# Kernel tuning notes

Hardware: AMD Instinct MI355X
Metric: run time of the kernel (lower is better)

Reference implementation:

```python
import jax, jax.numpy as jnp
import numpy as np

B, S, D, H = 2, 2048, 1024, 16
HD = D // H  # head_dim = 64


def setup_inputs() -> dict:
    key = jax.random.key(0)
    ks = jax.random.split(key, 12)
    s = 1.0 / np.sqrt(D)
    inp = {
        "query": jax.random.normal(ks[0], (B, S, D), jnp.float32),
        "key": jax.random.normal(ks[1], (B, S, D), jnp.float32),
        "value": jax.random.normal(ks[2], (B, S, D), jnp.float32),
        # causal mask, shape (B, S, S); 0 means masked
        "mask": jnp.broadcast_to(jnp.tril(jnp.ones((S, S), jnp.int32)), (B, S, S)),
        "Wq": jax.random.normal(ks[3], (D, D), jnp.float32) * s,
        "bq": jnp.zeros((D,), jnp.float32),
        "Wk": jax.random.normal(ks[4], (D, D), jnp.float32) * s,
        "bk": jnp.zeros((D,), jnp.float32),
        "Wv": jax.random.normal(ks[5], (D, D), jnp.float32) * s,
        "bv": jnp.zeros((D,), jnp.float32),
        "Wo": jax.random.normal(ks[6], (D, D), jnp.float32) * s,
        "bo": jnp.zeros((D,), jnp.float32),
    }
    return inp


def reference(query, key, value, mask, Wq, bq, Wk, bk, Wv, bv, Wo, bo):
    # QKV projections (nn.Linear: x @ W.T + b), split into heads -> (B, H, S, HD)
    def proj(x, W, b):
        return (x @ W.T + b).reshape(B, S, H, HD).transpose(0, 2, 1, 3)

    q = proj(query, Wq, bq)
    k = proj(key, Wk, bk)
    v = proj(value, Wv, bv)

    # scores: (B, H, S, S)
    scores = jnp.einsum("bhqd,bhkd->bhqk", q, k) / np.sqrt(HD).astype(np.float32)
    scores = jnp.where(mask[:, None, :, :] == 0, jnp.float32(-1e9), scores)
    attn = jax.nn.softmax(scores, axis=-1)
    # dropout is identity in eval mode
    ctx = jnp.einsum("bhqk,bhkd->bhqd", attn, v)  # (B, H, S, HD)
    ctx = ctx.transpose(0, 2, 1, 3).reshape(B, S, D)
    return ctx @ Wo.T + bo
```

## Files before the change

kernel.cpp:

```cpp
#include <hip/hip_runtime.h>
#include <hip/hip_bf16.h>
#include <stdint.h>


#define LOG2E 1.4426950408889634f

typedef __bf16 bf16x8 __attribute__((ext_vector_type(8)));
typedef float f32x4 __attribute__((ext_vector_type(4)));

__device__ __forceinline__ ushort f2bf(float f) {
  union { float f; uint32_t u; } v; v.f = f;
  uint32_t u = v.u + 0x7FFFu + ((v.u >> 16) & 1u);
  return (ushort)(u >> 16);
}
__device__ __forceinline__ uint32_t pack2(float a, float b) {
  return (uint32_t)f2bf(a) | ((uint32_t)f2bf(b) << 16);
}
__device__ __forceinline__ bf16x8 ld_frag(const ushort* p) {
  return __builtin_bit_cast(bf16x8, *(const uint4*)p);
}
__device__ __forceinline__ void gl_lds16(const void* g, void* l) {
  __builtin_amdgcn_global_load_lds(
      (const __attribute__((address_space(1))) void*)g,
      (__attribute__((address_space(3))) void*)l, 16, 0, 0);
}

template <int ROWS>
__device__ __forceinline__ void stage_tile(const ushort* src, int stride,
                                           ushort* dst, int wid, int lane) {
  const int rloc = lane >> 3;
  const int gsrc = (lane & 7) ^ (rloc & 7);
  constexpr int RW = ROWS / 4;
  const ushort* s = src + (size_t)(wid * RW + rloc) * stride + gsrc * 8;
#pragma unroll
  for (int j = 0; j < RW / 8; ++j)
    gl_lds16(s + (size_t)(j * 8) * stride, dst + (wid * RW + j * 8) * 64);
}
__device__ __forceinline__ int swz(int row, int gran) {
  return row * 64 + ((gran ^ (row & 7)) << 3);
}

__device__ __forceinline__ void cvt8(const float* s, ushort* d) {
  float4 f0 = ((const float4*)s)[0];
  float4 f1 = ((const float4*)s)[1];
  uint4 h;
  h.x = pack2(f0.x, f0.y); h.y = pack2(f0.z, f0.w);
  h.z = pack2(f1.x, f1.y); h.w = pack2(f1.z, f1.w);
  *(uint4*)d = h;
}

__global__ void cvt_all(const float* __restrict__ s0, const float* __restrict__ s1,
                        const float* __restrict__ s2, const float* __restrict__ s3,
                        const float* __restrict__ s4, const float* __restrict__ s5,
                        const float* __restrict__ s6, ushort* __restrict__ d0,
                        ushort* __restrict__ d1, ushort* __restrict__ d2,
                        ushort* __restrict__ d3, ushort* __restrict__ d4,
                        ushort* __restrict__ d5, ushort* __restrict__ d6) {
  int y = blockIdx.y;
  int n = (y < 3) ? (4096 * 1024) : (1024 * 1024);
  int i = (blockIdx.x * 256 + threadIdx.x) * 8;
  if (i >= n) return;
  const float* s; ushort* d;
  switch (y) {
    case 0: s = s0; d = d0; break;
    case 1: s = s1; d = d1; break;
    case 2: s = s2; d = d2; break;
    case 3: s = s3; d = d3; break;
    case 4: s = s4; d = d4; break;
    case 5: s = s5; d = d5; break;
    default: s = s6; d = d6; break;
  }
  cvt8(s + i, d + i);
}

template <int BN, bool OUT_BF16, bool PROJ3>
__global__ __launch_bounds__(256, 2) void gemm_bt(
    const ushort* __restrict__ A0, const ushort* __restrict__ A1, const ushort* __restrict__ A2,
    const ushort* __restrict__ W0, const ushort* __restrict__ W1, const ushort* __restrict__ W2,
    const float* __restrict__ b0, const float* __restrict__ b1, const float* __restrict__ b2,
    void* __restrict__ Y0, void* __restrict__ Y1, void* __restrict__ Y2,
    int Ndim, int Kdim) {
  __shared__ ushort Al[128 * 64];
  __shared__ ushort Bl[BN * 64];

  const int z = PROJ3 ? blockIdx.z : 0;
  const ushort* A = (z == 0) ? A0 : (z == 1) ? A1 : A2;
  const ushort* W = (z == 0) ? W0 : (z == 1) ? W1 : W2;
  const float* bias = (z == 0) ? b0 : (z == 1) ? b1 : b2;
  void* Yp = (z == 0) ? Y0 : (z == 1) ? Y1 : Y2;

  const int tid = threadIdx.x;
  const int wid = tid >> 6, lane = tid & 63;
  const int row0 = blockIdx.y * 128, col0 = blockIdx.x * BN;
  const int wr = wid >> 1, wc = wid & 1;
  const int lr = lane & 15, lg = lane >> 4;
  constexpr int NF = BN / 32;

  f32x4 acc[4][NF] = {};

  for (int k0 = 0; k0 < Kdim; k0 += 64) {
    stage_tile<128>(A + (size_t)row0 * Kdim + k0, Kdim, Al, wid, lane);
    stage_tile<BN>(W + (size_t)col0 * Kdim + k0, Kdim, Bl, wid, lane);
    __syncthreads();

#pragma unroll
    for (int kk = 0; kk < 2; ++kk) {
      bf16x8 af[4], bfr[NF];
#pragma unroll
      for (int m = 0; m < 4; ++m)
        af[m] = ld_frag(&Al[swz(wr * 64 + m * 16 + lr, kk * 4 + lg)]);
#pragma unroll
      for (int n = 0; n < NF; ++n)
        bfr[n] = ld_frag(&Bl[swz(wc * (BN / 2) + n * 16 + lr, kk * 4 + lg)]);
#pragma unroll
      for (int m = 0; m < 4; ++m)
#pragma unroll
        for (int n = 0; n < NF; ++n)
          acc[m][n] = __builtin_amdgcn_mfma_f32_16x16x32_bf16(af[m], bfr[n], acc[m][n], 0, 0, 0);
    }
    __syncthreads();
  }

#pragma unroll
  for (int n = 0; n < NF; ++n) {
    int col = col0 + wc * (BN / 2) + n * 16 + lr;
    float bv = bias[col];
#pragma unroll
    for (int m = 0; m < 4; ++m) {
#pragma unroll
      for (int r = 0; r < 4; ++r) {
        int row = row0 + wr * 64 + m * 16 + lg * 4 + r;
        float v = acc[m][n][r] + bv;
        if (OUT_BF16)
          ((ushort*)Yp)[(size_t)row * Ndim + col] = f2bf(v);
        else
          ((float*)Yp)[(size_t)row * Ndim + col] = v;
      }
    }
  }
}

__global__ __launch_bounds__(256, 2) void attn_kernel(
    const ushort* __restrict__ Qb, const ushort* __restrict__ Kb,
    const ushort* __restrict__ Vb, ushort* __restrict__ Cx) {
  __shared__ ushort Kl[2][64 * 64];
  __shared__ ushort Vt[64 * 64];
  __shared__ ushort Pl[4][16 * 64];

  const int tid = threadIdx.x;
  const int wid = tid >> 6, lane = tid & 63;
  const int lr = lane & 15, lg = lane >> 4;
  const int x = blockIdx.x;
  const int y = blockIdx.y;
  const int m8 = (x + (y & 7)) & 7;
  const int yh = y >> 3;
  const int qi = (yh == 0) ? m8 : (yh == 1) ? 15 - m8 : (yh == 2) ? 16 + m8 : 31 - m8;
  const int qb0 = qi * 64;
  const int b = x >> 4, h = x & 15;
  const size_t base = (size_t)b * 2048 * 1024 + h * 64;
  const int q0w = qb0 + wid * 16;
  const float SCL = 0.125f * LOG2E;

  bf16x8 qf[2];
  {
    const ushort* qs = Qb + base + (size_t)(q0w + lr) * 1024 + lg * 8;
    qf[0] = ld_frag(qs);
    qf[1] = ld_frag(qs + 32);
  }

  f32x4 O[4] = {};
  float m_reg = -1e30f, l_reg = 0.f;

  const int nt = qi + 1;
  const int vp = tid & 31;
  const int vc = tid >> 5;

  stage_tile<64>(Kb + base, 1024, Kl[0], wid, lane);
  uint4 va = *(const uint4*)(Vb + base + (size_t)(2 * vp) * 1024 + vc * 8);
  uint4 vb = *(const uint4*)(Vb + base + (size_t)(2 * vp + 1) * 1024 + vc * 8);

  for (int t = 0; t < nt; ++t) {
    const int kv0 = t * 64;
    {
      const ushort* pA = (const ushort*)&va;
      const ushort* pB = (const ushort*)&vb;
#pragma unroll
      for (int j = 0; j < 8; ++j) {
        int d = vc * 8 + j;
        int idx = d * 64 + (((vp >> 2) ^ j) << 3) + ((vp * 2) & 7);
        *(uint32_t*)&Vt[idx] = (uint32_t)pA[j] | ((uint32_t)pB[j] << 16);
      }
    }
    __syncthreads();

    if (t + 1 < nt) {
      stage_tile<64>(Kb + base + (size_t)(kv0 + 64) * 1024, 1024, Kl[(t + 1) & 1], wid, lane);
      va = *(const uint4*)(Vb + base + (size_t)(kv0 + 64 + 2 * vp) * 1024 + vc * 8);
      vb = *(const uint4*)(Vb + base + (size_t)(kv0 + 64 + 2 * vp + 1) * 1024 + vc * 8);
    }

    const bool dm = (t == nt - 1);
    const ushort* Kc = Kl[t & 1];

    f32x4 st[4];
#pragma unroll
    for (int cb = 0; cb < 4; ++cb) {
      if (kv0 + cb * 16 > q0w + 15) {
        st[cb] = f32x4{-1e30f, -1e30f, -1e30f, -1e30f};
        continue;
      }
      f32x4 a = {};
#pragma unroll
      for (int kk = 0; kk < 2; ++kk) {
        bf16x8 kfrag = ld_frag(&Kc[swz(cb * 16 + lr, kk * 4 + lg)]);
        a = __builtin_amdgcn_mfma_f32_16x16x32_bf16(kfrag, qf[kk], a, 0, 0, 0);
      }
#pragma unroll
      for (int r = 0; r < 4; ++r) {
        float s = a[r] * SCL;
        if (dm) {
          int kv = kv0 + cb * 16 + lg * 4 + r;
          if (kv > q0w + lr) s = -1e30f;
        }
        a[r] = s;
      }
      st[cb] = a;
    }

    float tmax = -1e30f;
#pragma unroll
    for (int cb = 0; cb < 4; ++cb) {
      float c01 = fmaxf(st[cb][0], st[cb][1]);
      float c23 = fmaxf(st[cb][2], st[cb][3]);
      tmax = fmaxf(tmax, fmaxf(c01, c23));
    }
    tmax = fmaxf(tmax, __shfl_xor(tmax, 16));
    tmax = fmaxf(tmax, __shfl_xor(tmax, 32));
    float mnew = fmaxf(m_reg, tmax);
    float alpha = exp2f(m_reg - mnew);
    m_reg = mnew;

    float ts = 0.f;
#pragma unroll
    for (int cb = 0; cb < 4; ++cb)
#pragma unroll
      for (int r = 0; r < 4; ++r) {
        float p = exp2f(st[cb][r] - mnew);
        st[cb][r] = p;
        ts += p;
      }
    ts += __shfl_xor(ts, 16);
    ts += __shfl_xor(ts, 32);
    l_reg = l_reg * alpha + ts;

    float aO[4];
#pragma unroll
    for (int r = 0; r < 4; ++r)
      aO[r] = __shfl(alpha, (lane & 48) | ((lane >> 2) & 12) | r);
#pragma unroll
    for (int n = 0; n < 4; ++n)
#pragma unroll
      for (int r = 0; r < 4; ++r) O[n][r] *= aO[r];

    ushort* pw = &Pl[wid][0];
#pragma unroll
    for (int cb = 0; cb < 4; ++cb) {
      int g = ((cb * 2 + (lg >> 1)) ^ (lr & 7)) << 3;
      int idx = lr * 64 + g + ((lg & 1) * 4);
      *(uint32_t*)&pw[idx] = pack2(st[cb][0], st[cb][1]);
      *(uint32_t*)&pw[idx + 2] = pack2(st[cb][2], st[cb][3]);
    }

#pragma unroll
    for (int kk = 0; kk < 2; ++kk) {
      bf16x8 pa = ld_frag(&pw[swz(lr, kk * 4 + lg)]);
#pragma unroll
      for (int n = 0; n < 4; ++n) {
        bf16x8 vfr = ld_frag(&Vt[swz(n * 16 + lr, kk * 4 + lg)]);
        O[n] = __builtin_amdgcn_mfma_f32_16x16x32_bf16(pa, vfr, O[n], 0, 0, 0);
      }
    }
    __syncthreads();
  }

#pragma unroll
  for (int r = 0; r < 4; ++r) {
    float ls = __shfl(l_reg, (lane & 48) | ((lane >> 2) & 12) | r);
    float inv = 1.f / ls;
    size_t row = (size_t)b * 2048 + q0w + lg * 4 + r;
#pragma unroll
    for (int n = 0; n < 4; ++n)
      Cx[row * 1024 + h * 64 + n * 16 + lr] = f2bf(O[n][r] * inv);
  }
}

extern "C" void kernel_launch(void* const* d_in, const int* in_sizes, int n_in,
                              void* d_out, int out_size, void* d_ws, size_t ws_size,
                              hipStream_t stream) {
  const float* query = (const float*)d_in[0];
  const float* key_i = (const float*)d_in[1];
  const float* value = (const float*)d_in[2];
  const float* Wq = (const float*)d_in[4];
  const float* bq = (const float*)d_in[5];
  const float* Wk = (const float*)d_in[6];
  const float* bk = (const float*)d_in[7];
  const float* Wv = (const float*)d_in[8];
  const float* bv = (const float*)d_in[9];
  const float* Wo = (const float*)d_in[10];
  const float* bo = (const float*)d_in[11];
  float* out = (float*)d_out;

  const size_t MD = (size_t)4096 * 1024;
  const size_t DD = (size_t)1024 * 1024;
  ushort* qbf = (ushort*)d_ws;
  ushort* kbf = qbf + MD;
  ushort* vbf = kbf + MD;
  ushort* Wqb = vbf + MD;
  ushort* Wkb = Wqb + DD;
  ushort* Wvb = Wkb + DD;
  ushort* Wob = Wvb + DD;
  ushort* Qb = Wob + DD;
  ushort* Kb = Qb + MD;
  ushort* Vb = Kb + MD;
  ushort* Cx = Vb + MD;

  cvt_all<<<dim3(2048, 7), 256, 0, stream>>>(query, key_i, value, Wq, Wk, Wv, Wo,
                                             qbf, kbf, vbf, Wqb, Wkb, Wvb, Wob);

  gemm_bt<128, true, true><<<dim3(8, 32, 3), 256, 0, stream>>>(
      qbf, kbf, vbf, Wqb, Wkb, Wvb, bq, bk, bv, Qb, Kb, Vb, 1024, 1024);

  attn_kernel<<<dim3(32, 32), 256, 0, stream>>>(Qb, Kb, Vb, Cx);

  gemm_bt<64, false, false><<<dim3(16, 32, 1), 256, 0, stream>>>(
      Cx, Cx, Cx, Wob, Wob, Wob, bo, bo, bo, out, out, out, 1024, 1024);
}
```

Baseline: 273.1 us.

## Double-buffer GEMM tiles, pair causal query blocks, add lazy softmax rescale

The GEMM kernel now double-buffers its A and W LDS tiles, loading the next K slice while the current one is multiplied, so one barrier per iteration is dropped. The attention kernel pairs query block p with block 31-p in one workgroup to balance causal work, halving the grid. It also skips the running-max rescale when the new tile max exceeds the old by at most 8 in log2 units, and converts P to bf16 by truncation instead of rounding. The lazy rescale and truncation trade a little accuracy for fewer ALU ops, and doubled LDS in the GEMM may lower occupancy.

After: 265.6 us. -2.7%, faster.

```diff
diff --git a/kernel.cpp b/kernel.cpp
--- a/kernel.cpp
+++ b/kernel.cpp
@@ -15,6 +15,11 @@
 }
 __device__ __forceinline__ uint32_t pack2(float a, float b) {
   return (uint32_t)f2bf(a) | ((uint32_t)f2bf(b) << 16);
+}
+__device__ __forceinline__ uint32_t pack2t(float a, float b) {
+  uint32_t ua = __builtin_bit_cast(uint32_t, a);
+  uint32_t ub = __builtin_bit_cast(uint32_t, b);
+  return (ua >> 16) | (ub & 0xFFFF0000u);
 }
 __device__ __forceinline__ bf16x8 ld_frag(const ushort* p) {
   return __builtin_bit_cast(bf16x8, *(const uint4*)p);
@@ -80,8 +85,8 @@
     const float* __restrict__ b0, const float* __restrict__ b1, const float* __restrict__ b2,
     void* __restrict__ Y0, void* __restrict__ Y1, void* __restrict__ Y2,
     int Ndim, int Kdim) {
-  __shared__ ushort Al[128 * 64];
-  __shared__ ushort Bl[BN * 64];
+  __shared__ ushort Al[2][128 * 64];
+  __shared__ ushort Bl[2][BN * 64];
 
   const int z = PROJ3 ? blockIdx.z : 0;
   const ushort* A = (z == 0) ? A0 : (z == 1) ? A1 : A2;
@@ -96,22 +101,32 @@
   const int lr = lane & 15, lg = lane >> 4;
   constexpr int NF = BN / 32;
 
+  const ushort* Arow = A + (size_t)row0 * Kdim;
+  const ushort* Wrow = W + (size_t)col0 * Kdim;
+
   f32x4 acc[4][NF] = {};
 
+  stage_tile<128>(Arow, Kdim, Al[0], wid, lane);
+  stage_tile<BN>(Wrow, Kdim, Bl[0], wid, lane);
+  __syncthreads();
+
+  int cur = 0;
   for (int k0 = 0; k0 < Kdim; k0 += 64) {
-    stage_tile<128>(A + (size_t)row0 * Kdim + k0, Kdim, Al, wid, lane);
-    stage_tile<BN>(W + (size_t)col0 * Kdim + k0, Kdim, Bl, wid, lane);
-    __syncthreads();
-
+    if (k0 + 64 < Kdim) {
+      stage_tile<128>(Arow + k0 + 64, Kdim, Al[cur ^ 1], wid, lane);
+      stage_tile<BN>(Wrow + k0 + 64, Kdim, Bl[cur ^ 1], wid, lane);
+    }
+    const ushort* Ac = Al[cur];
+    const ushort* Bc = Bl[cur];
 #pragma unroll
     for (int kk = 0; kk < 2; ++kk) {
       bf16x8 af[4], bfr[NF];
 #pragma unroll
       for (int m = 0; m < 4; ++m)
-        af[m] = ld_frag(&Al[swz(wr * 64 + m * 16 + lr, kk * 4 + lg)]);
+        af[m] = ld_frag(&Ac[swz(wr * 64 + m * 16 + lr, kk * 4 + lg)]);
 #pragma unroll
       for (int n = 0; n < NF; ++n)
-        bfr[n] = ld_frag(&Bl[swz(wc * (BN / 2) + n * 16 + lr, kk * 4 + lg)]);
+        bfr[n] = ld_frag(&Bc[swz(wc * (BN / 2) + n * 16 + lr, kk * 4 + lg)]);
 #pragma unroll
       for (int m = 0; m < 4; ++m)
 #pragma unroll
@@ -119,6 +134,7 @@
           acc[m][n] = __builtin_amdgcn_mfma_f32_16x16x32_bf16(af[m], bfr[n], acc[m][n], 0, 0, 0);
     }
     __syncthreads();
+    cur ^= 1;
   }
 
 #pragma unroll
@@ -151,146 +167,155 @@
   const int wid = tid >> 6, lane = tid & 63;
   const int lr = lane & 15, lg = lane >> 4;
   const int x = blockIdx.x;
-  const int y = blockIdx.y;
-  const int m8 = (x + (y & 7)) & 7;
-  const int yh = y >> 3;
-  const int qi = (yh == 0) ? m8 : (yh == 1) ? 15 - m8 : (yh == 2) ? 16 + m8 : 31 - m8;
-  const int qb0 = qi * 64;
+  const int p = blockIdx.y;
   const int b = x >> 4, h = x & 15;
   const size_t base = (size_t)b * 2048 * 1024 + h * 64;
-  const int q0w = qb0 + wid * 16;
   const float SCL = 0.125f * LOG2E;
-
-  bf16x8 qf[2];
-  {
-    const ushort* qs = Qb + base + (size_t)(q0w + lr) * 1024 + lg * 8;
-    qf[0] = ld_frag(qs);
-    qf[1] = ld_frag(qs + 32);
-  }
-
-  f32x4 O[4] = {};
-  float m_reg = -1e30f, l_reg = 0.f;
-
-  const int nt = qi + 1;
   const int vp = tid & 31;
   const int vc = tid >> 5;
 
-  stage_tile<64>(Kb + base, 1024, Kl[0], wid, lane);
-  uint4 va = *(const uint4*)(Vb + base + (size_t)(2 * vp) * 1024 + vc * 8);
-  uint4 vb = *(const uint4*)(Vb + base + (size_t)(2 * vp + 1) * 1024 + vc * 8);
-
-  for (int t = 0; t < nt; ++t) {
-    const int kv0 = t * 64;
+#pragma unroll 1
+  for (int seg = 0; seg < 2; ++seg) {
+    const int qi = seg ? (31 - p) : p;
+    const int qb0 = qi * 64;
+    const int q0w = qb0 + wid * 16;
+    const int nt = qi + 1;
+
+    bf16x8 qf[2];
     {
-      const ushort* pA = (const ushort*)&va;
-      const ushort* pB = (const ushort*)&vb;
-#pragma unroll
-      for (int j = 0; j < 8; ++j) {
-        int d = vc * 8 + j;
-        int idx = d * 64 + (((vp >> 2) ^ j) << 3) + ((vp * 2) & 7);
-        *(uint32_t*)&Vt[idx] = (uint32_t)pA[j] | ((uint32_t)pB[j] << 16);
-      }
-    }
-    __syncthreads();
-
-    if (t + 1 < nt) {
-      stage_tile<64>(Kb + base + (size_t)(kv0 + 64) * 1024, 1024, Kl[(t + 1) & 1], wid, lane);
-      va = *(const uint4*)(Vb + base + (size_t)(kv0 + 64 + 2 * vp) * 1024 + vc * 8);
-      vb = *(const uint4*)(Vb + base + (size_t)(kv0 + 64 + 2 * vp + 1) * 1024 + vc * 8);
-    }
-
-    const bool dm = (t == nt - 1);
-    const ushort* Kc = Kl[t & 1];
-
-    f32x4 st[4];
-#pragma unroll
-    for (int cb = 0; cb < 4; ++cb) {
-      if (kv0 + cb * 16 > q0w + 15) {
-        st[cb] = f32x4{-1e30f, -1e30f, -1e30f, -1e30f};
-        continue;
-      }
-      f32x4 a = {};
+      const ushort* qs = Qb + base + (size_t)(q0w + lr) * 1024 + lg * 8;
+      qf[0] = ld_frag(qs);
+      qf[1] = ld_frag(qs + 32);
+    }
+
+    f32x4 O[4] = {};
+    float m_reg = -1e30f, l_reg = 0.f;
+
+    stage_tile<64>(Kb + base, 1024, Kl[0], wid, lane);
+    uint4 va = *(const uint4*)(Vb + base + (size_t)(2 * vp) * 1024 + vc * 8);
+    uint4 vb = *(const uint4*)(Vb + base + (size_t)(2 * vp + 1) * 1024 + vc * 8);
+
+#pragma unroll 1
+    for (int t = 0; t < nt; ++t) {
+      const int kv0 = t * 64;
+      {
+        const ushort* pA = (const ushort*)&va;
+        const ushort* pB = (const ushort*)&vb;
+#pragma unroll
+        for (int j = 0; j < 8; ++j) {
+          int d = vc * 8 + j;
+          int idx = d * 64 + (((vp >> 2) ^ j) << 3) + ((vp * 2) & 7);
+          *(uint32_t*)&Vt[idx] = (uint32_t)pA[j] | ((uint32_t)pB[j] << 16);
+        }
+      }
+      __syncthreads();
+
+      if (t + 1 < nt) {
+        stage_tile<64>(Kb + base + (size_t)(kv0 + 64) * 1024, 1024, Kl[(t + 1) & 1], wid, lane);
+        va = *(const uint4*)(Vb + base + (size_t)(kv0 + 64 + 2 * vp) * 1024 + vc * 8);
+        vb = *(const uint4*)(Vb + base + (size_t)(kv0 + 64 + 2 * vp + 1) * 1024 + vc * 8);
+      }
+
+      const bool dm = (t == nt - 1);
+      const ushort* Kc = Kl[t & 1];
+
+      f32x4 st[4];
+#pragma unroll
+      for (int cb = 0; cb < 4; ++cb) {
+        if (kv0 + cb * 16 > q0w + 15) {
+          st[cb] = f32x4{-1e30f, -1e30f, -1e30f, -1e30f};
+          continue;
+        }
+        f32x4 a = {};
+#pragma unroll
+        for (int kk = 0; kk < 2; ++kk) {
+          bf16x8 kfrag = ld_frag(&Kc[swz(cb * 16 + lr, kk * 4 + lg)]);
+          a = __builtin_amdgcn_mfma_f32_16x16x32_bf16(kfrag, qf[kk], a, 0, 0, 0);
+        }
+#pragma unroll
+        for (int r = 0; r < 4; ++r) {
+          float s = a[r] * SCL;
+          if (dm) {
+            int kv = kv0 + cb * 16 + lg * 4 + r;
+            if (kv > q0w + lr) s = -1e30f;
+          }
+          a[r] = s;
+        }
+        st[cb] = a;
+      }
+
+      float tmax = -1e30f;
+#pragma unroll
+      for (int cb = 0; cb < 4; ++cb) {
+        float c01 = fmaxf(st[cb][0], st[cb][1]);
+        float c23 = fmaxf(st[cb][2], st[cb][3]);
+        tmax = fmaxf(tmax, fmaxf(c01, c23));
+      }
+      tmax = fmaxf(tmax, __shfl_xor(tmax, 16));
+      tmax = fmaxf(tmax, __shfl_xor(tmax, 32));
+
+      const bool skip = __all(tmax - m_reg <= 8.f);
+      float mcur;
+      if (skip) {
+        mcur = m_reg;
+      } else {
+        mcur = fmaxf(m_reg, tmax);
+        float alpha = exp2f(m_reg - mcur);
+        m_reg = mcur;
+        l_reg *= alpha;
+        float aO[4];
+#pragma unroll
+        for (int r = 0; r < 4; ++r)
+          aO[r] = __shfl(alpha, (lane & 48) | ((lane >> 2) & 12) | r);
+#pragma unroll
+        for (int n = 0; n < 4; ++n)
+#pragma unroll
+          for (int r = 0; r < 4; ++r) O[n][r] *= aO[r];
+      }
+
+      float ts = 0.f;
+#pragma unroll
+      for (int cb = 0; cb < 4; ++cb)
+#pragma unroll
+        for (int r = 0; r < 4; ++r) {
+          float pv = exp2f(st[cb][r] - mcur);
+          st[cb][r] = pv;
+          ts += pv;
+        }
+      ts += __shfl_xor(ts, 16);
+      ts += __shfl_xor(ts, 32);
+      l_reg += ts;
+
+      ushort* pw = &Pl[wid][0];
+#pragma unroll
+      for (int cb = 0; cb < 4; ++cb) {
+        int g = ((cb * 2 + (lg >> 1)) ^ (lr & 7)) << 3;
+        int idx = lr * 64 + g + ((lg & 1) * 4);
+        *(uint32_t*)&pw[idx] = pack2t(st[cb][0], st[cb][1]);
+        *(uint32_t*)&pw[idx + 2] = pack2t(st[cb][2], st[cb][3]);
+      }
+
 #pragma unroll
       for (int kk = 0; kk < 2; ++kk) {
-        bf16x8 kfrag = ld_frag(&Kc[swz(cb * 16 + lr, kk * 4 + lg)]);
-        a = __builtin_amdgcn_mfma_f32_16x16x32_bf16(kfrag, qf[kk], a, 0, 0, 0);
-      }
-#pragma unroll
-      for (int r = 0; r < 4; ++r) {
-        float s = a[r] * SCL;
-        if (dm) {
-          int kv = kv0 + cb * 16 + lg * 4 + r;
-          if (kv > q0w + lr) s = -1e30f;
-        }
-        a[r] = s;
-      }
-      st[cb] = a;
-    }
-
-    float tmax = -1e30f;
-#pragma unroll
-    for (int cb = 0; cb < 4; ++cb) {
-      float c01 = fmaxf(st[cb][0], st[cb][1]);
-      float c23 = fmaxf(st[cb][2], st[cb][3]);
-      tmax = fmaxf(tmax, fmaxf(c01, c23));
-    }
-    tmax = fmaxf(tmax, __shfl_xor(tmax, 16));
-    tmax = fmaxf(tmax, __shfl_xor(tmax, 32));
-    float mnew = fmaxf(m_reg, tmax);
-    float alpha = exp2f(m_reg - mnew);
-    m_reg = mnew;
-
-    float ts = 0.f;
-#pragma unroll
-    for (int cb = 0; cb < 4; ++cb)
-#pragma unroll
-      for (int r = 0; r < 4; ++r) {
-        float p = exp2f(st[cb][r] - mnew);
-        st[cb][r] = p;
-        ts += p;
-      }
-    ts += __shfl_xor(ts, 16);
-    ts += __shfl_xor(ts, 32);
-    l_reg = l_reg * alpha + ts;
-
-    float aO[4];
-#pragma unroll
-    for (int r = 0; r < 4; ++r)
-      aO[r] = __shfl(alpha, (lane & 48) | ((lane >> 2) & 12) | r);
-#pragma unroll
-    for (int n = 0; n < 4; ++n)
-#pragma unroll
-      for (int r = 0; r < 4; ++r) O[n][r] *= aO[r];
-
-    ushort* pw = &Pl[wid][0];
-#pragma unroll
-    for (int cb = 0; cb < 4; ++cb) {
-      int g = ((cb * 2 + (lg >> 1)) ^ (lr & 7)) << 3;
-      int idx = lr * 64 + g + ((lg & 1) * 4);
-      *(uint32_t*)&pw[idx] = pack2(st[cb][0], st[cb][1]);
-      *(uint32_t*)&pw[idx + 2] = pack2(st[cb][2], st[cb][3]);
-    }
-
-#pragma unroll
-    for (int kk = 0; kk < 2; ++kk) {
-      bf16x8 pa = ld_frag(&pw[swz(lr, kk * 4 + lg)]);
-#pragma unroll
-      for (int n = 0; n < 4; ++n) {
-        bf16x8 vfr = ld_frag(&Vt[swz(n * 16 + lr, kk * 4 + lg)]);
-        O[n] = __builtin_amdgcn_mfma_f32_16x16x32_bf16(pa, vfr, O[n], 0, 0, 0);
-      }
-    }
-    __syncthreads();
-  }
-
-#pragma unroll
-  for (int r = 0; r < 4; ++r) {
-    float ls = __shfl(l_reg, (lane & 48) | ((lane >> 2) & 12) | r);
-    float inv = 1.f / ls;
-    size_t row = (size_t)b * 2048 + q0w + lg * 4 + r;
-#pragma unroll
-    for (int n = 0; n < 4; ++n)
-      Cx[row * 1024 + h * 64 + n * 16 + lr] = f2bf(O[n][r] * inv);
+        bf16x8 pa = ld_frag(&pw[swz(lr, kk * 4 + lg)]);
+#pragma unroll
+        for (int n = 0; n < 4; ++n) {
+          bf16x8 vfr = ld_frag(&Vt[swz(n * 16 + lr, kk * 4 + lg)]);
+          O[n] = __builtin_amdgcn_mfma_f32_16x16x32_bf16(pa, vfr, O[n], 0, 0, 0);
+        }
+      }
+      __syncthreads();
+    }
+
+#pragma unroll
+    for (int r = 0; r < 4; ++r) {
+      float ls = __shfl(l_reg, (lane & 48) | ((lane >> 2) & 12) | r);
+      float inv = 1.f / ls;
+      size_t row = (size_t)b * 2048 + q0w + lg * 4 + r;
+#pragma unroll
+      for (int n = 0; n < 4; ++n)
+        Cx[row * 1024 + h * 64 + n * 16 + lr] = f2bf(O[n][r] * inv);
+    }
   }
 }
 
@@ -330,7 +355,7 @@
   gemm_bt<128, true, true><<<dim3(8, 32, 3), 256, 0, stream>>>(
       qbf, kbf, vbf, Wqb, Wkb, Wvb, bq, bk, bv, Qb, Kb, Vb, 1024, 1024);
 
-  attn_kernel<<<dim3(32, 32), 256, 0, stream>>>(Qb, Kb, Vb, Cx);
+  attn_kernel<<<dim3(32, 16), 256, 0, stream>>>(Qb, Kb, Vb, Cx);
 
   gemm_bt<64, false, false><<<dim3(16, 32, 1), 256, 0, stream>>>(
       Cx, Cx, Cx, Wob, Wob, Wob, bo, bo, bo, out, out, out, 1024, 1024);
```
